# Kernel optimization log

Hardware: AMD Instinct MI355X
Metric: run time of the kernel (lower is better)

Reference implementation:

```python
import jax, jax.numpy as jnp
import numpy as np

M = 4096   # nodes per layer (also number of input nodes)
L = 32     # internal layers
K = 64     # in-degree of each internal node


def setup_inputs() -> dict:
    key = jax.random.key(0)
    k_x, k_wi, k_bi, k_w, k_b, k_g = jax.random.split(key, 6)
    x = jax.random.normal(k_x, (M, 1), dtype=jnp.float32)
    w_in = jax.random.normal(k_wi, (M, 1), dtype=jnp.float32)
    b_in = jax.random.normal(k_bi, (M,), dtype=jnp.float32)
    # scale internal weights so sigmoid(K-term dot) is not fully saturated
    w = jax.random.normal(k_w, (L, M, K), dtype=jnp.float32) * 0.05
    b = jax.random.normal(k_b, (L, M), dtype=jnp.float32)
    # predecessor indices into the previous layer's value vector
    igraf = jax.random.randint(k_g, (L, M, K), 0, M, dtype=jnp.int32)
    return {"x": x, "w_in": w_in, "b_in": b_in, "w": w, "b": b, "igraf": igraf}


def reference(x, w_in, b_in, w, b, igraf):
    # input nodes: relu(Linear(1,1)) applied to each scalar input, vectorized
    v = jax.nn.relu(w_in[:, 0] * x[:, 0] + b_in)          # [M]
    # internal nodes, layer by layer (topological order):
    # each node gathers K predecessor values and applies sigmoid(Linear(K,1))
    for l in range(L):
        g = v[igraf[l]]                                   # [M, K] irregular gather
        v = jax.nn.sigmoid(jnp.einsum('mk,mk->m', w[l], g) + b[l])
    # original returns values[n_nodes - 1] (shape [1])
    return v[-1:]
```

## Files before the change

### kernel.cpp

```cpp
#include <hip/hip_runtime.h>

#define M 4096
#define L 32
#define K 64
#define NBLK 256
#define BLOCK 256
#define NPW 4
#define NPB 16
#define MK (M * K)
#define FB 0xAAAAAAAAu

__global__ __launch_bounds__(BLOCK)
void net_kernel(const float* __restrict__ x,
                const float* __restrict__ w_in,
                const float* __restrict__ b_in,
                const float* __restrict__ w,
                const float* __restrict__ b,
                const int* __restrict__ igraf,
                float* __restrict__ out,
                unsigned long long* __restrict__ buf)
{
    __shared__ float sv[M];

    const int tid  = threadIdx.x;
    const int blk  = blockIdx.x;
    const int wave = tid >> 6;
    const int lane = tid & 63;
    const int base = blk * NPB + wave * NPW;
    const bool lastblk = (blk == NBLK - 1);

    float wv[NPW]; int iv[NPW]; float breg = 0.0f;
    {
        const size_t b0 = (size_t)base * K + (size_t)lane;
        #pragma unroll
        for (int j = 0; j < NPW; ++j) {
            wv[j] = w[b0 + (size_t)j * K];
            iv[j] = igraf[b0 + (size_t)j * K];
        }
        if (lane < NPW) breg = b[base + lane];
    }

    #pragma unroll
    for (int j = 0; j < 4; ++j) {
        const int idx = tid + j * BLOCK;
        const float4 x4 = ((const float4*)x)[idx];
        const float4 wi = ((const float4*)w_in)[idx];
        const float4 bi = ((const float4*)b_in)[idx];
        float4 r;
        r.x = fmaxf(fmaf(wi.x, x4.x, bi.x), 0.0f);
        r.y = fmaxf(fmaf(wi.y, x4.y, bi.y), 0.0f);
        r.z = fmaxf(fmaf(wi.z, x4.z, bi.z), 0.0f);
        r.w = fmaxf(fmaf(wi.w, x4.w, bi.w), 0.0f);
        ((float4*)sv)[idx] = r;
    }
    __syncthreads();

    for (int l = 0; l < L; ++l) {
        float p[NPW];
        #pragma unroll
        for (int j = 0; j < NPW; ++j) p[j] = wv[j] * sv[iv[j]];

        #pragma unroll
        for (int j = 0; j < NPW; ++j) {
            #pragma unroll
            for (int off = 32; off > 0; off >>= 1)
                p[j] += __shfl_xor(p[j], off, 64);
        }

        float pj = p[0];
        pj = (lane == 1) ? p[1] : pj;
        pj = (lane == 2) ? p[2] : pj;
        pj = (lane == 3) ? p[3] : pj;
        const float val = 1.0f / (1.0f + __expf(-(pj + breg)));

        if (l == L - 1) {
            if (wave == 3 && lane == 3) out[0] = val;
            break;
        }

        const unsigned tag = FB + (unsigned)(l + 1);
        unsigned long long* bufr = buf + (size_t)((l + 1) & 1) * M;

        if (lane < NPW) {
            const unsigned long long pk =
                ((unsigned long long)tag << 32) |
                (unsigned long long)__float_as_uint(val);
            __hip_atomic_store(&bufr[base + lane], pk,
                               __ATOMIC_RELAXED, __HIP_MEMORY_SCOPE_AGENT);
        }

        if ((l == L - 2) && !lastblk) return;

        if ((l + 2 < L) || lastblk) {
            const size_t nb = (size_t)(l + 1) * MK + (size_t)base * K + (size_t)lane;
            #pragma unroll
            for (int j = 0; j < NPW; ++j) {
                wv[j] = w[nb + (size_t)j * K];
                iv[j] = igraf[nb + (size_t)j * K];
            }
            if (lane < NPW) breg = b[(l + 1) * M + base + lane];
        }

        unsigned long long vals[16];
        #pragma unroll
        for (int j = 0; j < 16; ++j)
            vals[j] = __hip_atomic_load(&bufr[tid + j * BLOCK],
                                        __ATOMIC_RELAXED,
                                        __HIP_MEMORY_SCOPE_AGENT);

        __syncthreads();

        for (;;) {
            bool ok = true;
            #pragma unroll
            for (int j = 0; j < 16; ++j) {
                if ((unsigned)(vals[j] >> 32) != tag) {
                    ok = false;
                    vals[j] = __hip_atomic_load(&bufr[tid + j * BLOCK],
                                                __ATOMIC_RELAXED,
                                                __HIP_MEMORY_SCOPE_AGENT);
                }
            }
            if (ok) break;
            __builtin_amdgcn_s_sleep(1);
        }

        #pragma unroll
        for (int j = 0; j < 16; ++j)
            sv[tid + j * BLOCK] = __uint_as_float((unsigned)vals[j]);
        __syncthreads();
    }
}

extern "C" void kernel_launch(void* const* d_in, const int* in_sizes, int n_in,
                              void* d_out, int out_size, void* d_ws, size_t ws_size,
                              hipStream_t stream) {
    const float* x     = (const float*)d_in[0];
    const float* w_in  = (const float*)d_in[1];
    const float* b_in  = (const float*)d_in[2];
    const float* wt    = (const float*)d_in[3];
    const float* b     = (const float*)d_in[4];
    const int*   igraf = (const int*)d_in[5];
    float*       out   = (float*)d_out;

    unsigned long long* buf = (unsigned long long*)d_ws;

    hipLaunchKernelGGL(net_kernel, dim3(NBLK), dim3(BLOCK), 0, stream,
                       x, w_in, b_in, wt, b, igraf, out, buf);
    (void)in_sizes; (void)n_in; (void)out_size; (void)ws_size;
}
```

Before: 179.4 us.

## Gather predecessors directly from global tagged buffer, drop block-wide layer broadcast

Result: slower. 194.3 us (+8.3%).

```diff
diff --git a/kernel.cpp b/kernel.cpp
--- a/kernel.cpp
+++ b/kernel.cpp
@@ -31,11 +31,11 @@
 
     float wv[NPW]; int iv[NPW]; float breg = 0.0f;
     {
-        const size_t b0 = (size_t)base * K + (size_t)lane;
+        const size_t f0 = (size_t)base * K + (size_t)lane;
         #pragma unroll
         for (int j = 0; j < NPW; ++j) {
-            wv[j] = w[b0 + (size_t)j * K];
-            iv[j] = igraf[b0 + (size_t)j * K];
+            wv[j] = w[f0 + (size_t)j * K];
+            iv[j] = igraf[f0 + (size_t)j * K];
         }
         if (lane < NPW) breg = b[base + lane];
     }
@@ -55,80 +55,89 @@
     }
     __syncthreads();
 
-    for (int l = 0; l < L; ++l) {
-        float p[NPW];
-        #pragma unroll
-        for (int j = 0; j < NPW; ++j) p[j] = wv[j] * sv[iv[j]];
-
-        #pragma unroll
-        for (int j = 0; j < NPW; ++j) {
+    for (int t = 0; t < L; ++t) {
+        unsigned long long gv[NPW];
+        const unsigned long long* src = buf + (size_t)(t - 1) * M;
+        if (t > 0) {
             #pragma unroll
-            for (int off = 32; off > 0; off >>= 1)
-                p[j] += __shfl_xor(p[j], off, 64);
+            for (int j = 0; j < NPW; ++j)
+                gv[j] = __hip_atomic_load(&src[iv[j]], __ATOMIC_RELAXED,
+                                          __HIP_MEMORY_SCOPE_AGENT);
         }
 
-        float pj = p[0];
-        pj = (lane == 1) ? p[1] : pj;
-        pj = (lane == 2) ? p[2] : pj;
-        pj = (lane == 3) ? p[3] : pj;
-        const float val = 1.0f / (1.0f + __expf(-(pj + breg)));
+        float nwv[NPW]; int niv[NPW]; float nbreg = 0.0f;
+        const bool pf = (t + 1 < L - 1) || (t + 1 == L - 1 && lastblk);
+        if (pf) {
+            const size_t nb = (size_t)(t + 1) * MK + (size_t)base * K + (size_t)lane;
+            #pragma unroll
+            for (int j = 0; j < NPW; ++j) {
+                nwv[j] = w[nb + (size_t)j * K];
+                niv[j] = igraf[nb + (size_t)j * K];
+            }
+            if (lane < NPW) nbreg = b[(t + 1) * M + base + lane];
+        }
 
-        if (l == L - 1) {
+        float p0, p1, p2, p3;
+        if (t == 0) {
+            p0 = wv[0] * sv[iv[0]];
+            p1 = wv[1] * sv[iv[1]];
+            p2 = wv[2] * sv[iv[2]];
+            p3 = wv[3] * sv[iv[3]];
+        } else {
+            const unsigned tag = FB + (unsigned)t;
+            for (;;) {
+                bool ok = true;
+                #pragma unroll
+                for (int j = 0; j < NPW; ++j) {
+                    if ((unsigned)(gv[j] >> 32) != tag) {
+                        ok = false;
+                        gv[j] = __hip_atomic_load(&src[iv[j]], __ATOMIC_RELAXED,
+                                                  __HIP_MEMORY_SCOPE_AGENT);
+                    }
+                }
+                if (ok) break;
+            }
+            p0 = wv[0] * __uint_as_float((unsigned)gv[0]);
+            p1 = wv[1] * __uint_as_float((unsigned)gv[1]);
+            p2 = wv[2] * __uint_as_float((unsigned)gv[2]);
+            p3 = wv[3] * __uint_as_float((unsigned)gv[3]);
+        }
+
+        const bool m0 = (lane & 1) != 0;
+        float u  = m0 ? p1 : p0;
+        float uv = m0 ? p0 : p1;
+        u += __shfl_xor(uv, 1, 64);
+        float wq = m0 ? p3 : p2;
+        float wz = m0 ? p2 : p3;
+        wq += __shfl_xor(wz, 1, 64);
+        const bool m1 = (lane & 2) != 0;
+        float q  = m1 ? wq : u;
+        float qr = m1 ? u : wq;
+        q += __shfl_xor(qr, 2, 64);
+        #pragma unroll
+        for (int off = 4; off < 64; off <<= 1)
+            q += __shfl_xor(q, off, 64);
+
+        const float val = 1.0f / (1.0f + __expf(-(q + breg)));
+
+        if (t == L - 1) {
             if (wave == 3 && lane == 3) out[0] = val;
             break;
         }
 
-        const unsigned tag = FB + (unsigned)(l + 1);
-        unsigned long long* bufr = buf + (size_t)((l + 1) & 1) * M;
-
         if (lane < NPW) {
             const unsigned long long pk =
-                ((unsigned long long)tag << 32) |
+                ((unsigned long long)(FB + (unsigned)(t + 1)) << 32) |
                 (unsigned long long)__float_as_uint(val);
-            __hip_atomic_store(&bufr[base + lane], pk,
+            __hip_atomic_store(&buf[(size_t)t * M + base + lane], pk,
                                __ATOMIC_RELAXED, __HIP_MEMORY_SCOPE_AGENT);
         }
 
-        if ((l == L - 2) && !lastblk) return;
-
-        if ((l + 2 < L) || lastblk) {
-            const size_t nb = (size_t)(l + 1) * MK + (size_t)base * K + (size_t)lane;
-            #pragma unroll
-            for (int j = 0; j < NPW; ++j) {
-                wv[j] = w[nb + (size_t)j * K];
-                iv[j] = igraf[nb + (size_t)j * K];
-            }
-            if (lane < NPW) breg = b[(l + 1) * M + base + lane];
-        }
-
-        unsigned long long vals[16];
-        #pragma unroll
-        for (int j = 0; j < 16; ++j)
-            vals[j] = __hip_atomic_load(&bufr[tid + j * BLOCK],
-                                        __ATOMIC_RELAXED,
-                                        __HIP_MEMORY_SCOPE_AGENT);
-
-        __syncthreads();
-
-        for (;;) {
-            bool ok = true;
-            #pragma unroll
-            for (int j = 0; j < 16; ++j) {
-                if ((unsigned)(vals[j] >> 32) != tag) {
-                    ok = false;
-                    vals[j] = __hip_atomic_load(&bufr[tid + j * BLOCK],
-                                                __ATOMIC_RELAXED,
-                                                __HIP_MEMORY_SCOPE_AGENT);
-                }
-            }
-            if (ok) break;
-            __builtin_amdgcn_s_sleep(1);
-        }
+        if (t == L - 2 && !lastblk) return;
 
         #pragma unroll
-        for (int j = 0; j < 16; ++j)
-            sv[tid + j * BLOCK] = __uint_as_float((unsigned)vals[j]);
-        __syncthreads();
+        for (int j = 0; j < NPW; ++j) { wv[j] = nwv[j]; iv[j] = niv[j]; }
+        breg = nbreg;
     }
 }
 
```

## Use 64 blocks with four threads per node and per-layer exchange buffers

Applied to the files above, without the earlier changes.

New measurement: 160.3 us. 10.6% less time.

```diff
diff --git a/kernel.cpp b/kernel.cpp
--- a/kernel.cpp
+++ b/kernel.cpp
@@ -3,11 +3,10 @@
 #define M 4096
 #define L 32
 #define K 64
-#define NBLK 256
+#define NBLK 64
 #define BLOCK 256
-#define NPW 4
-#define NPB 16
-#define MK (M * K)
+#define NPB 64
+#define EPT 16
 #define FB 0xAAAAAAAAu
 
 __global__ __launch_bounds__(BLOCK)
@@ -22,22 +21,21 @@
 {
     __shared__ float sv[M];
 
-    const int tid  = threadIdx.x;
-    const int blk  = blockIdx.x;
-    const int wave = tid >> 6;
-    const int lane = tid & 63;
-    const int base = blk * NPB + wave * NPW;
+    const int tid   = threadIdx.x;
+    const int blk   = blockIdx.x;
+    const int node  = blk * NPB + (tid >> 2);
+    const int chunk = tid & 3;
+    const bool pub  = (chunk == 0);
     const bool lastblk = (blk == NBLK - 1);
 
-    float wv[NPW]; int iv[NPW]; float breg = 0.0f;
+    float4 wv[4]; int4 iv[4]; float breg = 0.0f;
     {
-        const size_t b0 = (size_t)base * K + (size_t)lane;
-        #pragma unroll
-        for (int j = 0; j < NPW; ++j) {
-            wv[j] = w[b0 + (size_t)j * K];
-            iv[j] = igraf[b0 + (size_t)j * K];
-        }
-        if (lane < NPW) breg = b[base + lane];
+        const size_t f0 = (size_t)node * K + (size_t)chunk * EPT;
+        const float4* wp = (const float4*)(w + f0);
+        const int4*   ip = (const int4*)(igraf + f0);
+        wv[0] = wp[0]; wv[1] = wp[1]; wv[2] = wp[2]; wv[3] = wp[3];
+        iv[0] = ip[0]; iv[1] = ip[1]; iv[2] = ip[2]; iv[3] = ip[3];
+        if (pub) breg = b[node];
     }
 
     #pragma unroll
@@ -55,74 +53,69 @@
     }
     __syncthreads();
 
-    for (int l = 0; l < L; ++l) {
-        float p[NPW];
+    for (int t = 0; t < L; ++t) {
+        float p = 0.0f;
         #pragma unroll
-        for (int j = 0; j < NPW; ++j) p[j] = wv[j] * sv[iv[j]];
+        for (int q = 0; q < 4; ++q) {
+            p = fmaf(wv[q].x, sv[iv[q].x], p);
+            p = fmaf(wv[q].y, sv[iv[q].y], p);
+            p = fmaf(wv[q].z, sv[iv[q].z], p);
+            p = fmaf(wv[q].w, sv[iv[q].w], p);
+        }
+        p += __shfl_xor(p, 1, 64);
+        p += __shfl_xor(p, 2, 64);
 
-        #pragma unroll
-        for (int j = 0; j < NPW; ++j) {
-            #pragma unroll
-            for (int off = 32; off > 0; off >>= 1)
-                p[j] += __shfl_xor(p[j], off, 64);
-        }
+        float val = 0.0f;
+        if (pub) val = 1.0f / (1.0f + __expf(-(p + breg)));
 
-        float pj = p[0];
-        pj = (lane == 1) ? p[1] : pj;
-        pj = (lane == 2) ? p[2] : pj;
-        pj = (lane == 3) ? p[3] : pj;
-        const float val = 1.0f / (1.0f + __expf(-(pj + breg)));
-
-        if (l == L - 1) {
-            if (wave == 3 && lane == 3) out[0] = val;
+        if (t == L - 1) {
+            if (tid == 252) out[0] = val;
             break;
         }
 
-        const unsigned tag = FB + (unsigned)(l + 1);
-        unsigned long long* bufr = buf + (size_t)((l + 1) & 1) * M;
-
-        if (lane < NPW) {
+        if (pub) {
             const unsigned long long pk =
-                ((unsigned long long)tag << 32) |
+                ((unsigned long long)(FB + (unsigned)(t + 1)) << 32) |
                 (unsigned long long)__float_as_uint(val);
-            __hip_atomic_store(&bufr[base + lane], pk,
+            __hip_atomic_store(&buf[(size_t)t * M + node], pk,
                                __ATOMIC_RELAXED, __HIP_MEMORY_SCOPE_AGENT);
         }
 
-        if ((l == L - 2) && !lastblk) return;
+        if (t == L - 2 && !lastblk) return;
 
-        if ((l + 2 < L) || lastblk) {
-            const size_t nb = (size_t)(l + 1) * MK + (size_t)base * K + (size_t)lane;
-            #pragma unroll
-            for (int j = 0; j < NPW; ++j) {
-                wv[j] = w[nb + (size_t)j * K];
-                iv[j] = igraf[nb + (size_t)j * K];
-            }
-            if (lane < NPW) breg = b[(l + 1) * M + base + lane];
+        {
+            const size_t nb = ((size_t)(t + 1) * M + (size_t)node) * K
+                            + (size_t)chunk * EPT;
+            const float4* wp = (const float4*)(w + nb);
+            const int4*   ip = (const int4*)(igraf + nb);
+            wv[0] = wp[0]; wv[1] = wp[1]; wv[2] = wp[2]; wv[3] = wp[3];
+            iv[0] = ip[0]; iv[1] = ip[1]; iv[2] = ip[2]; iv[3] = ip[3];
+            if (pub) breg = b[(t + 1) * M + node];
         }
 
+        const unsigned long long* src = buf + (size_t)t * M;
         unsigned long long vals[16];
         #pragma unroll
         for (int j = 0; j < 16; ++j)
-            vals[j] = __hip_atomic_load(&bufr[tid + j * BLOCK],
+            vals[j] = __hip_atomic_load(&src[tid + j * BLOCK],
                                         __ATOMIC_RELAXED,
                                         __HIP_MEMORY_SCOPE_AGENT);
 
         __syncthreads();
 
+        const unsigned tag = FB + (unsigned)(t + 1);
         for (;;) {
             bool ok = true;
             #pragma unroll
             for (int j = 0; j < 16; ++j) {
                 if ((unsigned)(vals[j] >> 32) != tag) {
                     ok = false;
-                    vals[j] = __hip_atomic_load(&bufr[tid + j * BLOCK],
+                    vals[j] = __hip_atomic_load(&src[tid + j * BLOCK],
                                                 __ATOMIC_RELAXED,
                                                 __HIP_MEMORY_SCOPE_AGENT);
                 }
             }
             if (ok) break;
-            __builtin_amdgcn_s_sleep(1);
         }
 
         #pragma unroll
```
